# Performance work log

Hardware: AMD Instinct MI355X
Metric: run time of the kernel (lower is better)

The kernel has to match this reference:

```python
import jax, jax.numpy as jnp
import numpy as np


def setup_inputs() -> dict:
    key = jax.random.key(0)
    ks = jax.random.split(key, 4)
    B, S, D, U = 4, 4096, 128, 64
    x = jax.random.normal(ks[0], (B, S, D), dtype=jnp.float32)
    Wq = jax.random.normal(ks[1], (D, U), dtype=jnp.float32) * (1.0 / np.sqrt(D))
    Wk = jax.random.normal(ks[2], (D, U), dtype=jnp.float32) * (1.0 / np.sqrt(D))
    Wv = jax.random.normal(ks[3], (D, U), dtype=jnp.float32) * (1.0 / np.sqrt(D))
    bq = jnp.zeros((U,), dtype=jnp.float32)
    bk = jnp.zeros((U,), dtype=jnp.float32)
    bv = jnp.zeros((U,), dtype=jnp.float32)
    return {"x": x, "Wq": Wq, "bq": bq, "Wk": Wk, "bk": bk, "Wv": Wv, "bv": bv}


def reference(x, Wq, bq, Wk, bk, Wv, bv):
    # Single-head, unscaled, unmasked attention (faithful to the Keras layer).
    q = jnp.einsum("bsd,du->bsu", x, Wq) + bq  # [B,S,U]
    k = jnp.einsum("bsd,du->bsu", x, Wk) + bk  # [B,S,U]
    v = jnp.einsum("bsd,du->bsu", x, Wv) + bv  # [B,S,U]
    scores = jnp.einsum("bsu,btu->bst", q, k)  # [B,S,S], no 1/sqrt(d) scaling
    attn = jax.nn.softmax(scores, axis=-1)
    return jnp.einsum("bst,btu->bsu", attn, v)  # [B,S,U]
```

## Files before the change

### kernel.cpp

```cpp
#include <hip/hip_runtime.h>
#include <hip/hip_fp16.h>
#include <math.h>

#define SEQ   4096
#define DIM   128
#define UDIM  64
#define BATCH 4
#define BS    (BATCH*SEQ)

typedef _Float16 h8 __attribute__((ext_vector_type(8)));
typedef _Float16 h4 __attribute__((ext_vector_type(4)));
typedef _Float16 h2 __attribute__((ext_vector_type(2)));
typedef float    f4 __attribute__((ext_vector_type(4)));

#define MFMA_K32(a,b,c) __builtin_amdgcn_mfma_f32_16x16x32_f16((a),(b),(c),0,0,0)
#define MFMA_K16(a,b,c) __builtin_amdgcn_mfma_f32_16x16x16f16((a),(b),(c),0,0,0)

__device__ __forceinline__ h2 pk2(float a, float b) {
  return __builtin_bit_cast(h2, __builtin_amdgcn_cvt_pkrtz(a, b));
}

#define WT_STRIDE 272
#define VB_STRIDE 144
#define L2E 1.44269504088896f

__global__ __launch_bounds__(256, 3) void proj_mfma(
    const float* __restrict__ x,
    const float* __restrict__ Wq, const float* __restrict__ bq,
    const float* __restrict__ Wk, const float* __restrict__ bk,
    const float* __restrict__ Wv, const float* __restrict__ bv,
    _Float16* __restrict__ qf, _Float16* __restrict__ kf, _Float16* __restrict__ vt)
{
  const int proj = blockIdx.y;
  const float* __restrict__ W    = proj==0 ? Wq : (proj==1 ? Wk : Wv);
  const float* __restrict__ bias = proj==0 ? bq : (proj==1 ? bk : bv);
  const int tid  = threadIdx.x;
  const int lane = tid & 63, wv = tid >> 6;
  const int n = lane & 15, quad = lane >> 4;
  const int r0 = blockIdx.x * 64;

  __shared__ __align__(16) char lds[UDIM * WT_STRIDE];

  #pragma unroll
  for (int i = 0; i < 8; ++i) {
    const int idx = i*256 + tid;
    const int nn  = idx & 63;
    const int k4  = (idx >> 6) * 4;
    const float w0 = W[(k4+0)*UDIM + nn];
    const float w1 = W[(k4+1)*UDIM + nn];
    const float w2 = W[(k4+2)*UDIM + nn];
    const float w3 = W[(k4+3)*UDIM + nn];
    int2 wd;
    wd.x = __builtin_bit_cast(int, pk2(w0, w1));
    wd.y = __builtin_bit_cast(int, pk2(w2, w3));
    *(int2*)(lds + nn*WT_STRIDE + k4*2) = wd;
  }
  __syncthreads();

  const int row = r0 + wv*16 + n;
  h8 xa[4];
  #pragma unroll
  for (int ks = 0; ks < 4; ++ks) {
    const float* xp = x + (size_t)row*DIM + ks*32 + quad*8;
    const f4 a = *(const f4*)xp, b = *(const f4*)(xp + 4);
    int4 pkd;
    pkd.x = __builtin_bit_cast(int, pk2(a[0], a[1]));
    pkd.y = __builtin_bit_cast(int, pk2(a[2], a[3]));
    pkd.z = __builtin_bit_cast(int, pk2(b[0], b[1]));
    pkd.w = __builtin_bit_cast(int, pk2(b[2], b[3]));
    xa[ks] = __builtin_bit_cast(h8, pkd);
  }

  f4 acc[4];
  #pragma unroll
  for (int nt = 0; nt < 4; ++nt) acc[nt] = (f4){0.f,0.f,0.f,0.f};

  #pragma unroll
  for (int ks = 0; ks < 4; ++ks)
    #pragma unroll
    for (int nt = 0; nt < 4; ++nt) {
      const h8 wf = *(const h8*)(lds + (nt*16 + n)*WT_STRIDE + (ks*32 + quad*8)*2);
      acc[nt] = MFMA_K32(xa[ks], wf, acc[nt]);
    }

  #pragma unroll
  for (int nt = 0; nt < 4; ++nt) {
    const float bb = bias[nt*16 + n];
    #pragma unroll
    for (int r = 0; r < 4; ++r) acc[nt][r] += bb;
  }

  if (proj < 2) {
    _Float16* __restrict__ out = (proj == 0) ? qf : kf;
    const int par = lane & 1;
    const unsigned sel = par ? 0x03020706u : 0x05040100u;
    #pragma unroll
    for (int nt = 0; nt < 4; ++nt)
      #pragma unroll
      for (int p = 0; p < 2; ++p) {
        const int r = 2*p;
        unsigned A  = __builtin_bit_cast(unsigned, pk2(acc[nt][r], acc[nt][r+1]));
        unsigned Bs = (unsigned)__builtin_amdgcn_mov_dpp((int)A, 0xB1, 0xF, 0xF, true);
        unsigned w  = __builtin_amdgcn_perm(Bs, A, sel);
        const int orow = r0 + wv*16 + 4*quad + r + par;
        const int ocol = nt*16 + n - par;
        *(unsigned*)((char*)out + ((size_t)orow*UDIM + ocol)*2) = w;
      }
  } else {
    __syncthreads();
    #pragma unroll
    for (int nt = 0; nt < 4; ++nt)
      #pragma unroll
      for (int p = 0; p < 2; ++p) {
        const int r = 2*p;
        const int u = nt*16 + n;
        const int lrow = wv*16 + 4*quad + r;
        *(unsigned*)(lds + u*VB_STRIDE + lrow*2) =
            __builtin_bit_cast(unsigned, pk2(acc[nt][r], acc[nt][r+1]));
      }
    __syncthreads();
    const int b  = r0 / SEQ;
    const int s0 = r0 % SEQ;
    #pragma unroll
    for (int i = 0; i < 2; ++i) {
      const int e = tid + 256*i;
      const int u = e >> 3, ch = e & 7;
      h8 v = *(const h8*)(lds + u*VB_STRIDE + ch*16);
      *(h8*)(vt + ((size_t)b*UDIM + u)*SEQ + s0 + ch*8) = v;
    }
  }
}

__global__ __launch_bounds__(256, 3) void flash_attn_t(
    const _Float16* __restrict__ qf, const _Float16* __restrict__ kf,
    const _Float16* __restrict__ vt,
    _Float16* __restrict__ opart, float* __restrict__ Mp, float* __restrict__ Lp,
    int nkt)
{
  const int qt = blockIdx.x, b = blockIdx.y, sp = blockIdx.z;
  const _Float16* __restrict__ qb = qf + (size_t)b*SEQ*UDIM;
  const _Float16* __restrict__ kb = kf + (size_t)b*SEQ*UDIM;
  const _Float16* __restrict__ vb = vt + (size_t)b*UDIM*SEQ;

  __shared__ __align__(16) char Ks[2][64 * VB_STRIDE];
  __shared__ __align__(16) char Vs[2][64 * VB_STRIDE];

  const int tid = threadIdx.x;
  const int lane = tid & 63, wv = tid >> 6;
  const int n = lane & 15, quad = lane >> 4;
  const int qbase = qt*128 + wv*32;

  h8 qB[2][2];
  #pragma unroll
  for (int nt = 0; nt < 2; ++nt)
    #pragma unroll
    for (int ks = 0; ks < 2; ++ks)
      qB[nt][ks] = *(const h8*)(qb + (size_t)(qbase + nt*16 + n)*UDIM + ks*32 + quad*8);

  f4 O[4][2], Ol[2];
  #pragma unroll
  for (int ut = 0; ut < 4; ++ut)
    #pragma unroll
    for (int nt = 0; nt < 2; ++nt) O[ut][nt] = (f4){0.f,0.f,0.f,0.f};
  Ol[0] = (f4){0.f,0.f,0.f,0.f};
  Ol[1] = (f4){0.f,0.f,0.f,0.f};

  float M[2] = {-1e30f, -1e30f};

  h4 ones_a;
  { const _Float16 o = (_Float16)1.0f;
    ones_a[0]=o; ones_a[1]=o; ones_a[2]=o; ones_a[3]=o; }

  const int e0 = tid, e1 = tid + 256;
  const _Float16* kg0 = kb + ((size_t)sp*nkt*64 + (e0>>3))*UDIM + (e0&7)*8;
  const _Float16* kg1 = kb + ((size_t)sp*nkt*64 + (e1>>3))*UDIM + (e1&7)*8;
  const _Float16* vg0 = vb + (size_t)(e0>>3)*SEQ + sp*nkt*64 + (e0&7)*8;
  const _Float16* vg1 = vb + (size_t)(e1>>3)*SEQ + sp*nkt*64 + (e1&7)*8;
  const int kofs0 = (e0>>3)*VB_STRIDE + (e0&7)*16;
  const int kofs1 = (e1>>3)*VB_STRIDE + (e1&7)*16;

  h8 pk0 = *(const h8*)kg0, pk1 = *(const h8*)kg1;
  h8 pv0 = *(const h8*)vg0, pv1 = *(const h8*)vg1;
  *(h8*)(Ks[0]+kofs0) = pk0;  *(h8*)(Ks[0]+kofs1) = pk1;
  *(h8*)(Vs[0]+kofs0) = pv0;  *(h8*)(Vs[0]+kofs1) = pv1;
  __syncthreads();

  for (int kt = 0; kt < nkt; ++kt) {
    const int cur = kt & 1;
    const bool more = (kt + 1 < nkt);
    const char* __restrict__ Kc = Ks[cur];
    const char* __restrict__ Vc = Vs[cur];

    if (more) {
      kg0 += (size_t)64*UDIM;  kg1 += (size_t)64*UDIM;
      vg0 += 64;               vg1 += 64;
      pk0 = *(const h8*)kg0;   pk1 = *(const h8*)kg1;
      pv0 = *(const h8*)vg0;   pv1 = *(const h8*)vg1;
    }

    f4 S[4][2];
    #pragma unroll
    for (int mt = 0; mt < 4; ++mt)
      #pragma unroll
      for (int nt = 0; nt < 2; ++nt) S[mt][nt] = (f4){0.f,0.f,0.f,0.f};

    #pragma unroll
    for (int ks = 0; ks < 2; ++ks) {
      h8 ka[4];
      #pragma unroll
      for (int mt = 0; mt < 4; ++mt)
        ka[mt] = *(const h8*)(Kc + (mt*16 + n)*VB_STRIDE + ks*64 + quad*16);
      #pragma unroll
      for (int mt = 0; mt < 4; ++mt)
        #pragma unroll
        for (int nt = 0; nt < 2; ++nt)
          S[mt][nt] = MFMA_K32(ka[mt], qB[nt][ks], S[mt][nt]);
    }

    float alpha[2];
    #pragma unroll
    for (int nt = 0; nt < 2; ++nt) {
      float rm = S[0][nt][0];
      #pragma unroll
      for (int mt = 0; mt < 4; ++mt)
        #pragma unroll
        for (int r = 0; r < 4; ++r) rm = fmaxf(rm, S[mt][nt][r]);
      rm = fmaxf(rm, __shfl_xor(rm, 16));
      rm = fmaxf(rm, __shfl_xor(rm, 32));
      const float mo = M[nt];
      const float mn = fmaxf(mo, rm);
      alpha[nt] = exp2f((mo - mn) * L2E);
      const float mnl = mn * L2E;
      #pragma unroll
      for (int mt = 0; mt < 4; ++mt)
        #pragma unroll
        for (int r = 0; r < 4; ++r)
          S[mt][nt][r] = exp2f(fmaf(S[mt][nt][r], L2E, -mnl));
      M[nt] = mn;
      #pragma unroll
      for (int ut = 0; ut < 4; ++ut)
        #pragma unroll
        for (int r = 0; r < 4; ++r) O[ut][nt][r] *= alpha[nt];
      #pragma unroll
      for (int r = 0; r < 4; ++r) Ol[nt][r] *= alpha[nt];
    }

    h4 pB[4][2];
    #pragma unroll
    for (int mt = 0; mt < 4; ++mt)
      #pragma unroll
      for (int nt = 0; nt < 2; ++nt) {
        int2 t;
        t.x = __builtin_bit_cast(int, pk2(S[mt][nt][0], S[mt][nt][1]));
        t.y = __builtin_bit_cast(int, pk2(S[mt][nt][2], S[mt][nt][3]));
        pB[mt][nt] = __builtin_bit_cast(h4, t);
      }

    #pragma unroll
    for (int mt = 0; mt < 4; ++mt) {
      h4 va[4];
      #pragma unroll
      for (int ut = 0; ut < 4; ++ut)
        va[ut] = *(const h4*)(Vc + (ut*16 + n)*VB_STRIDE + mt*32 + quad*8);
      #pragma unroll
      for (int ut = 0; ut < 4; ++ut)
        #pragma unroll
        for (int nt = 0; nt < 2; ++nt)
          O[ut][nt] = MFMA_K16(va[ut], pB[mt][nt], O[ut][nt]);
      #pragma unroll
      for (int nt = 0; nt < 2; ++nt)
        Ol[nt] = MFMA_K16(ones_a, pB[mt][nt], Ol[nt]);
    }

    if (more) {
      char* __restrict__ Kn = Ks[cur ^ 1];
      char* __restrict__ Vn = Vs[cur ^ 1];
      *(h8*)(Kn+kofs0) = pk0;  *(h8*)(Kn+kofs1) = pk1;
      *(h8*)(Vn+kofs0) = pv0;  *(h8*)(Vn+kofs1) = pv1;
      __syncthreads();
    }
  }

  const size_t rowg = (size_t)sp*BS + (size_t)b*SEQ + qbase;
  #pragma unroll
  for (int nt = 0; nt < 2; ++nt) {
    char* __restrict__ orow = (char*)(opart + (rowg + nt*16 + n)*UDIM);
    #pragma unroll
    for (int ut = 0; ut < 4; ++ut)
      #pragma unroll
      for (int p = 0; p < 2; ++p)
        *(unsigned*)(orow + (ut*16 + quad*4 + 2*p)*2) =
            __builtin_bit_cast(unsigned, pk2(O[ut][nt][2*p], O[ut][nt][2*p+1]));
    if (quad == 0) {
      Mp[rowg + nt*16 + n] = M[nt] * L2E;
      Lp[rowg + nt*16 + n] = Ol[nt][0];
    }
  }
}

__global__ __launch_bounds__(256) void merge_out(
    const _Float16* __restrict__ opart, const float* __restrict__ Mp,
    const float* __restrict__ Lp, float* __restrict__ out, int nsplit)
{
  const int tid = threadIdx.x;
  const int row = blockIdx.x*16 + (tid >> 4);
  const int u4  = (tid & 15) * 4;
  float M = -1e30f;
  for (int s = 0; s < nsplit; ++s) M = fmaxf(M, Mp[(size_t)s*BS + row]);
  f4 num = (f4){0.f,0.f,0.f,0.f};
  float den = 0.f;
  for (int s = 0; s < nsplit; ++s) {
    const float w = exp2f(Mp[(size_t)s*BS + row] - M);
    den += w * Lp[(size_t)s*BS + row];
    const h4 op = *(const h4*)(opart + ((size_t)s*BS + row)*UDIM + u4);
    #pragma unroll
    for (int i = 0; i < 4; ++i) num[i] += w * (float)op[i];
  }
  const float dinv = 1.f / den;
  *(f4*)(out + (size_t)row*UDIM + u4) = num * dinv;
}

extern "C" void kernel_launch(void* const* d_in, const int* in_sizes, int n_in,
                              void* d_out, int out_size, void* d_ws, size_t ws_size,
                              hipStream_t stream) {
  (void)in_sizes; (void)n_in; (void)out_size;
  const float* x  = (const float*)d_in[0];
  const float* Wq = (const float*)d_in[1];
  const float* bq = (const float*)d_in[2];
  const float* Wk = (const float*)d_in[3];
  const float* bk = (const float*)d_in[4];
  const float* Wv = (const float*)d_in[5];
  const float* bv = (const float*)d_in[6];
  float* out = (float*)d_out;

  char* ws = (char*)d_ws;
  const size_t fBytes = (size_t)BS * UDIM * 2;
  auto need = [](int nsp) {
    return (size_t)3*BS*UDIM*2 + (size_t)nsp*BS*4*2 + (size_t)nsp*BS*UDIM*2;
  };
  int nsplit;
  if      (ws_size >= need(8)) nsplit = 8;
  else if (ws_size >= need(4)) nsplit = 4;
  else if (ws_size >= need(2)) nsplit = 2;
  else                         nsplit = 1;

  _Float16* qf = (_Float16*)(ws);
  _Float16* kf = (_Float16*)(ws + fBytes);
  _Float16* vt = (_Float16*)(ws + 2*fBytes);
  float* Mp    = (float*)(ws + 3*fBytes);
  float* Lp    = (float*)(ws + 3*fBytes + (size_t)nsplit*BS*4);
  _Float16* opart = (_Float16*)(ws + 3*fBytes + (size_t)nsplit*BS*8);

  proj_mfma<<<dim3(BS/64, 3), 256, 0, stream>>>(x, Wq, bq, Wk, bk, Wv, bv, qf, kf, vt);
  flash_attn_t<<<dim3(SEQ/128, BATCH, nsplit), 256, 0, stream>>>(
      qf, kf, vt, opart, Mp, Lp, (SEQ/64)/nsplit);
  merge_out<<<dim3(BS/16), 256, 0, stream>>>(opart, Mp, Lp, out, nsplit);
}
```

Measured before the change: 121.1 us.

## Pre-swizzle K/V into MFMA fragment layout and drop LDS staging in attention

The projection kernel now writes K and V directly in per-lane MFMA fragment order, so the attention kernel can load its operands straight from global memory with coalesced vector loads. This removes the LDS double buffer and the block barriers. The attention kernel shrinks to one wave per block (32 query rows), which gives 4x more blocks, and it software-prefetches the next V fragment. exp2f is also swapped for the hardware exp2 builtin. In exchange, every wave re-reads K/V from L2 with no sharing across waves in a block, which raises global/L2 traffic.

Result: slower. 127.9 us (+5.6%).

```diff
diff --git a/kernel.cpp b/kernel.cpp
--- a/kernel.cpp
+++ b/kernel.cpp
@@ -20,16 +20,25 @@
   return __builtin_bit_cast(h2, __builtin_amdgcn_cvt_pkrtz(a, b));
 }
 
+__device__ __forceinline__ float fexp2(float x) {
+#if __has_builtin(__builtin_amdgcn_exp2f)
+  return __builtin_amdgcn_exp2f(x);
+#else
+  return exp2f(x);
+#endif
+}
+
 #define WT_STRIDE 272
-#define VB_STRIDE 144
+#define KB_STRIDE 144
 #define L2E 1.44269504088896f
+
 
 __global__ __launch_bounds__(256, 3) void proj_mfma(
     const float* __restrict__ x,
     const float* __restrict__ Wq, const float* __restrict__ bq,
     const float* __restrict__ Wk, const float* __restrict__ bk,
     const float* __restrict__ Wv, const float* __restrict__ bv,
-    _Float16* __restrict__ qf, _Float16* __restrict__ kf, _Float16* __restrict__ vt)
+    _Float16* __restrict__ qf, _Float16* __restrict__ kswz, _Float16* __restrict__ vswz)
 {
   const int proj = blockIdx.y;
   const float* __restrict__ W    = proj==0 ? Wq : (proj==1 ? Wk : Wv);
@@ -40,6 +49,7 @@
   const int r0 = blockIdx.x * 64;
 
   __shared__ __align__(16) char lds[UDIM * WT_STRIDE];
+  __shared__ __align__(16) char kbnc[4 * 16 * KB_STRIDE];
 
   #pragma unroll
   for (int i = 0; i < 8; ++i) {
@@ -90,8 +100,10 @@
     for (int r = 0; r < 4; ++r) acc[nt][r] += bb;
   }
 
-  if (proj < 2) {
-    _Float16* __restrict__ out = (proj == 0) ? qf : kf;
+  const int b  = r0 / SEQ;
+  const int kb = ((r0 % SEQ) >> 4) + wv;
+
+  if (proj == 0) {
     const int par = lane & 1;
     const unsigned sel = par ? 0x03020706u : 0x05040100u;
     #pragma unroll
@@ -104,51 +116,48 @@
         unsigned w  = __builtin_amdgcn_perm(Bs, A, sel);
         const int orow = r0 + wv*16 + 4*quad + r + par;
         const int ocol = nt*16 + n - par;
-        *(unsigned*)((char*)out + ((size_t)orow*UDIM + ocol)*2) = w;
+        *(unsigned*)((char*)qf + ((size_t)orow*UDIM + ocol)*2) = w;
       }
+  } else if (proj == 1) {
+    char* base = kbnc + wv*(16*KB_STRIDE);
+    #pragma unroll
+    for (int nt = 0; nt < 4; ++nt)
+      #pragma unroll
+      for (int r = 0; r < 4; ++r)
+        *(_Float16*)(base + (4*quad + r)*KB_STRIDE + (nt*16 + n)*2) =
+            (_Float16)acc[nt][r];
+    _Float16* kdst = kswz + (size_t)b*SEQ*UDIM;
+    #pragma unroll
+    for (int ks = 0; ks < 2; ++ks) {
+      const h8 f = *(const h8*)(base + n*KB_STRIDE + ks*64 + quad*16);
+      *(h8*)(kdst + ((size_t)(kb*2 + ks)*64 + lane)*8) = f;
+    }
   } else {
-    __syncthreads();
-    #pragma unroll
-    for (int nt = 0; nt < 4; ++nt)
-      #pragma unroll
-      for (int p = 0; p < 2; ++p) {
-        const int r = 2*p;
-        const int u = nt*16 + n;
-        const int lrow = wv*16 + 4*quad + r;
-        *(unsigned*)(lds + u*VB_STRIDE + lrow*2) =
-            __builtin_bit_cast(unsigned, pk2(acc[nt][r], acc[nt][r+1]));
-      }
-    __syncthreads();
-    const int b  = r0 / SEQ;
-    const int s0 = r0 % SEQ;
-    #pragma unroll
-    for (int i = 0; i < 2; ++i) {
-      const int e = tid + 256*i;
-      const int u = e >> 3, ch = e & 7;
-      h8 v = *(const h8*)(lds + u*VB_STRIDE + ch*16);
-      *(h8*)(vt + ((size_t)b*UDIM + u)*SEQ + s0 + ch*8) = v;
-    }
-  }
-}
-
-__global__ __launch_bounds__(256, 3) void flash_attn_t(
-    const _Float16* __restrict__ qf, const _Float16* __restrict__ kf,
-    const _Float16* __restrict__ vt,
+    _Float16* vdst = vswz + (size_t)b*SEQ*UDIM;
+    #pragma unroll
+    for (int nt = 0; nt < 4; ++nt) {
+      int2 t;
+      t.x = __builtin_bit_cast(int, pk2(acc[nt][0], acc[nt][1]));
+      t.y = __builtin_bit_cast(int, pk2(acc[nt][2], acc[nt][3]));
+      *(int2*)(vdst + ((size_t)(kb*4 + nt)*64 + lane)*4) = t;
+    }
+  }
+}
+
+__global__ __launch_bounds__(64, 4) void flash_attn_t(
+    const _Float16* __restrict__ qf, const _Float16* __restrict__ kswz,
+    const _Float16* __restrict__ vswz,
     _Float16* __restrict__ opart, float* __restrict__ Mp, float* __restrict__ Lp,
     int nkt)
 {
   const int qt = blockIdx.x, b = blockIdx.y, sp = blockIdx.z;
-  const _Float16* __restrict__ qb = qf + (size_t)b*SEQ*UDIM;
-  const _Float16* __restrict__ kb = kf + (size_t)b*SEQ*UDIM;
-  const _Float16* __restrict__ vb = vt + (size_t)b*UDIM*SEQ;
-
-  __shared__ __align__(16) char Ks[2][64 * VB_STRIDE];
-  __shared__ __align__(16) char Vs[2][64 * VB_STRIDE];
-
-  const int tid = threadIdx.x;
-  const int lane = tid & 63, wv = tid >> 6;
+  const _Float16* __restrict__ qb = qf   + (size_t)b*SEQ*UDIM;
+  const _Float16* __restrict__ kz = kswz + (size_t)b*SEQ*UDIM;
+  const _Float16* __restrict__ vz = vswz + (size_t)b*SEQ*UDIM;
+
+  const int lane = threadIdx.x & 63;
   const int n = lane & 15, quad = lane >> 4;
-  const int qbase = qt*128 + wv*32;
+  const int qbase = qt * 32;
 
   h8 qB[2][2];
   #pragma unroll
@@ -171,32 +180,8 @@
   { const _Float16 o = (_Float16)1.0f;
     ones_a[0]=o; ones_a[1]=o; ones_a[2]=o; ones_a[3]=o; }
 
-  const int e0 = tid, e1 = tid + 256;
-  const _Float16* kg0 = kb + ((size_t)sp*nkt*64 + (e0>>3))*UDIM + (e0&7)*8;
-  const _Float16* kg1 = kb + ((size_t)sp*nkt*64 + (e1>>3))*UDIM + (e1&7)*8;
-  const _Float16* vg0 = vb + (size_t)(e0>>3)*SEQ + sp*nkt*64 + (e0&7)*8;
-  const _Float16* vg1 = vb + (size_t)(e1>>3)*SEQ + sp*nkt*64 + (e1&7)*8;
-  const int kofs0 = (e0>>3)*VB_STRIDE + (e0&7)*16;
-  const int kofs1 = (e1>>3)*VB_STRIDE + (e1&7)*16;
-
-  h8 pk0 = *(const h8*)kg0, pk1 = *(const h8*)kg1;
-  h8 pv0 = *(const h8*)vg0, pv1 = *(const h8*)vg1;
-  *(h8*)(Ks[0]+kofs0) = pk0;  *(h8*)(Ks[0]+kofs1) = pk1;
-  *(h8*)(Vs[0]+kofs0) = pv0;  *(h8*)(Vs[0]+kofs1) = pv1;
-  __syncthreads();
-
-  for (int kt = 0; kt < nkt; ++kt) {
-    const int cur = kt & 1;
-    const bool more = (kt + 1 < nkt);
-    const char* __restrict__ Kc = Ks[cur];
-    const char* __restrict__ Vc = Vs[cur];
-
-    if (more) {
-      kg0 += (size_t)64*UDIM;  kg1 += (size_t)64*UDIM;
-      vg0 += 64;               vg1 += 64;
-      pk0 = *(const h8*)kg0;   pk1 = *(const h8*)kg1;
-      pv0 = *(const h8*)vg0;   pv1 = *(const h8*)vg1;
-    }
+  for (int t = 0; t < nkt; ++t) {
+    const int kb0 = (sp*nkt + t) * 4;
 
     f4 S[4][2];
     #pragma unroll
@@ -209,13 +194,18 @@
       h8 ka[4];
       #pragma unroll
       for (int mt = 0; mt < 4; ++mt)
-        ka[mt] = *(const h8*)(Kc + (mt*16 + n)*VB_STRIDE + ks*64 + quad*16);
+        ka[mt] = *(const h8*)(kz + ((size_t)((kb0 + mt)*2 + ks)*64 + lane)*8);
       #pragma unroll
       for (int mt = 0; mt < 4; ++mt)
         #pragma unroll
         for (int nt = 0; nt < 2; ++nt)
           S[mt][nt] = MFMA_K32(ka[mt], qB[nt][ks], S[mt][nt]);
     }
+
+    h4 vcur[4], vnext[4];
+    #pragma unroll
+    for (int ut = 0; ut < 4; ++ut)
+      vcur[ut] = *(const h4*)(vz + ((size_t)(kb0*4 + ut)*64 + lane)*4);
 
     float alpha[2];
     #pragma unroll
@@ -229,13 +219,13 @@
       rm = fmaxf(rm, __shfl_xor(rm, 32));
       const float mo = M[nt];
       const float mn = fmaxf(mo, rm);
-      alpha[nt] = exp2f((mo - mn) * L2E);
+      alpha[nt] = fexp2((mo - mn) * L2E);
       const float mnl = mn * L2E;
       #pragma unroll
       for (int mt = 0; mt < 4; ++mt)
         #pragma unroll
         for (int r = 0; r < 4; ++r)
-          S[mt][nt][r] = exp2f(fmaf(S[mt][nt][r], L2E, -mnl));
+          S[mt][nt][r] = fexp2(fmaf(S[mt][nt][r], L2E, -mnl));
       M[nt] = mn;
       #pragma unroll
       for (int ut = 0; ut < 4; ++ut)
@@ -250,34 +240,29 @@
     for (int mt = 0; mt < 4; ++mt)
       #pragma unroll
       for (int nt = 0; nt < 2; ++nt) {
-        int2 t;
-        t.x = __builtin_bit_cast(int, pk2(S[mt][nt][0], S[mt][nt][1]));
-        t.y = __builtin_bit_cast(int, pk2(S[mt][nt][2], S[mt][nt][3]));
-        pB[mt][nt] = __builtin_bit_cast(h4, t);
+        int2 tt;
+        tt.x = __builtin_bit_cast(int, pk2(S[mt][nt][0], S[mt][nt][1]));
+        tt.y = __builtin_bit_cast(int, pk2(S[mt][nt][2], S[mt][nt][3]));
+        pB[mt][nt] = __builtin_bit_cast(h4, tt);
       }
 
     #pragma unroll
     for (int mt = 0; mt < 4; ++mt) {
-      h4 va[4];
+      if (mt < 3) {
+        #pragma unroll
+        for (int ut = 0; ut < 4; ++ut)
+          vnext[ut] = *(const h4*)(vz + ((size_t)((kb0 + mt + 1)*4 + ut)*64 + lane)*4);
+      }
       #pragma unroll
       for (int ut = 0; ut < 4; ++ut)
-        va[ut] = *(const h4*)(Vc + (ut*16 + n)*VB_STRIDE + mt*32 + quad*8);
-      #pragma unroll
-      for (int ut = 0; ut < 4; ++ut)
         #pragma unroll
         for (int nt = 0; nt < 2; ++nt)
-          O[ut][nt] = MFMA_K16(va[ut], pB[mt][nt], O[ut][nt]);
+          O[ut][nt] = MFMA_K16(vcur[ut], pB[mt][nt], O[ut][nt]);
       #pragma unroll
       for (int nt = 0; nt < 2; ++nt)
         Ol[nt] = MFMA_K16(ones_a, pB[mt][nt], Ol[nt]);
-    }
-
-    if (more) {
-      char* __restrict__ Kn = Ks[cur ^ 1];
-      char* __restrict__ Vn = Vs[cur ^ 1];
-      *(h8*)(Kn+kofs0) = pk0;  *(h8*)(Kn+kofs1) = pk1;
-      *(h8*)(Vn+kofs0) = pv0;  *(h8*)(Vn+kofs1) = pv1;
-      __syncthreads();
+      #pragma unroll
+      for (int ut = 0; ut < 4; ++ut) vcur[ut] = vnext[ut];
     }
   }
 
@@ -310,7 +295,7 @@
   f4 num = (f4){0.f,0.f,0.f,0.f};
   float den = 0.f;
   for (int s = 0; s < nsplit; ++s) {
-    const float w = exp2f(Mp[(size_t)s*BS + row] - M);
+    const float w = fexp2(Mp[(size_t)s*BS + row] - M);
     den += w * Lp[(size_t)s*BS + row];
     const h4 op = *(const h4*)(opart + ((size_t)s*BS + row)*UDIM + u4);
     #pragma unroll
@@ -344,15 +329,15 @@
   else if (ws_size >= need(2)) nsplit = 2;
   else                         nsplit = 1;
 
-  _Float16* qf = (_Float16*)(ws);
-  _Float16* kf = (_Float16*)(ws + fBytes);
-  _Float16* vt = (_Float16*)(ws + 2*fBytes);
-  float* Mp    = (float*)(ws + 3*fBytes);
-  float* Lp    = (float*)(ws + 3*fBytes + (size_t)nsplit*BS*4);
+  _Float16* qf   = (_Float16*)(ws);
+  _Float16* kswz = (_Float16*)(ws + fBytes);
+  _Float16* vswz = (_Float16*)(ws + 2*fBytes);
+  float* Mp      = (float*)(ws + 3*fBytes);
+  float* Lp      = (float*)(ws + 3*fBytes + (size_t)nsplit*BS*4);
   _Float16* opart = (_Float16*)(ws + 3*fBytes + (size_t)nsplit*BS*8);
 
-  proj_mfma<<<dim3(BS/64, 3), 256, 0, stream>>>(x, Wq, bq, Wk, bk, Wv, bv, qf, kf, vt);
-  flash_attn_t<<<dim3(SEQ/128, BATCH, nsplit), 256, 0, stream>>>(
-      qf, kf, vt, opart, Mp, Lp, (SEQ/64)/nsplit);
+  proj_mfma<<<dim3(BS/64, 3), 256, 0, stream>>>(x, Wq, bq, Wk, bk, Wv, bv, qf, kswz, vswz);
+  flash_attn_t<<<dim3(SEQ/32, BATCH, nsplit), 64, 0, stream>>>(
+      qf, kswz, vswz, opart, Mp, Lp, (SEQ/64)/nsplit);
   merge_out<<<dim3(BS/16), 256, 0, stream>>>(opart, Mp, Lp, out, nsplit);
 }
```
